# Kernel optimization log

Measured on AMD Instinct MI355X. Metric: run time of the kernel, lower is better.

Reference implementation:

```python
import jax, jax.numpy as jnp
import numpy as np

B, T, DIM, H = 2, 2048, 2048, 16
HD = DIM // H  # 128
ROPE_BASE = 10000.0


def _rope_angles(seq_len, head_dim, offset=0, dtype=jnp.float32):
    inv_freq = 1.0 / (ROPE_BASE ** (jnp.arange(0, head_dim, 2, dtype=dtype) / head_dim))
    pos = jnp.arange(offset, offset + seq_len, dtype=dtype)
    ang = pos[:, None] * inv_freq[None, :]              # [T, HD/2]
    ang = jnp.concatenate([ang, ang], axis=-1)          # [T, HD]
    return jnp.cos(ang), jnp.sin(ang)


def _rotate_half(x):
    x1, x2 = jnp.split(x, 2, axis=-1)
    return jnp.concatenate([-x2, x1], axis=-1)


def setup_inputs() -> dict:
    key = jax.random.key(0)
    ks = jax.random.split(key, 5)
    s = 0.02
    return {
        "x": jax.random.normal(ks[0], (B, T, DIM), dtype=jnp.float32),
        "Wq": jax.random.normal(ks[1], (DIM, DIM), dtype=jnp.float32) * s,
        "Wk": jax.random.normal(ks[2], (DIM, HD), dtype=jnp.float32) * s,
        "Wv": jax.random.normal(ks[3], (DIM, HD), dtype=jnp.float32) * s,
        "Wo": jax.random.normal(ks[4], (DIM, DIM), dtype=jnp.float32) * s,
    }


def reference(x, Wq, Wk, Wv, Wo):
    # q: [B, H, T, HD]; k, v: single shared head [B, T, HD]
    q = (x @ Wq).reshape(B, T, H, HD).transpose(0, 2, 1, 3)
    k = x @ Wk
    v = x @ Wv

    # RoPE (offset=0, no kv cache)
    cos, sin = _rope_angles(T, HD, 0, x.dtype)
    q = q * cos[None, None] + _rotate_half(q) * sin[None, None]
    k = k * cos[None] + _rotate_half(k) * sin[None]

    present_k = k[:, None]  # [B, 1, T, HD]
    present_v = v[:, None]

    # MQA attention: broadcast shared KV head via einsum (no materialized expand)
    scale = 1.0 / jnp.sqrt(jnp.asarray(HD, x.dtype))
    scores = jnp.einsum('bhqd,bkd->bhqk', q, k) * scale  # [B, H, T, T]
    causal = jnp.tril(jnp.ones((T, T), dtype=bool))
    scores = jnp.where(causal[None, None], scores, jnp.finfo(scores.dtype).min)
    attn = jax.nn.softmax(scores, axis=-1)
    out = jnp.einsum('bhqk,bkd->bhqd', attn, v)          # [B, H, T, HD]
    out = out.transpose(0, 2, 1, 3).reshape(B, T, DIM) @ Wo
    return (out, present_k, present_v)
```

## Files before the change

### kernel.cpp

```cpp
#include <hip/hip_runtime.h>


typedef __attribute__((ext_vector_type(8))) short short8;
typedef __attribute__((ext_vector_type(4))) float float4v;
typedef __attribute__((ext_vector_type(4))) unsigned short ushort4v;

#define LOG2E 1.4426950408889634f
#define ATT_SCALE 0.08838834764831845f
#define RLOG 0.20762050593046014f

__device__ __forceinline__ float bf2f(ushort u) {
    union { unsigned u; float f; } v; v.u = ((unsigned)u) << 16; return v.f;
}
__device__ __forceinline__ ushort f2bf(float f) {
    union { float f; unsigned u; } v; v.f = f;
    return (ushort)((v.u + 0x7FFF + ((v.u >> 16) & 1)) >> 16);
}
__device__ __forceinline__ ushort f2bf_fast(float f) {
    union { float f; unsigned u; } v; v.f = f;
    return (ushort)((v.u + 0x8000u) >> 16);
}
__device__ __forceinline__ float4v mfma16(short8 a, short8 b, float4v c) {
    return __builtin_amdgcn_mfma_f32_16x16x32_bf16(a, b, c, 0, 0, 0);
}
__device__ __forceinline__ void gl_lds16(const ushort* g, ushort* l) {
    __builtin_amdgcn_global_load_lds(
        (const __attribute__((address_space(1))) unsigned int*)g,
        (__attribute__((address_space(3))) unsigned int*)l, 16, 0, 0);
}

__global__ __launch_bounds__(256) void prep(const float* __restrict__ x,
                                            ushort* __restrict__ x_bf,
                                            float* __restrict__ tbl) {
    int bid = blockIdx.x;
    if (bid < 512) {
        int idx = bid * 256 + threadIdx.x;
        int d = idx & 63, t = idx >> 6;
        float inv = exp2f(-(float)d * RLOG);
        float s, c;
        sincosf((float)t * inv, &s, &c);
        tbl[idx * 2] = c;  tbl[idx * 2 + 1] = s;
    } else {
        int i = ((bid - 512) * 256 + threadIdx.x) * 4;
        float4v v = *(const float4v*)&x[i];
        ushort4v u;
        #pragma unroll
        for (int r = 0; r < 4; ++r) u[r] = f2bf(v[r]);
        *(ushort4v*)&x_bf[i] = u;
    }
}

__global__ __launch_bounds__(256) void transpose_cvt(const float* __restrict__ in,
                                                     ushort* __restrict__ out,
                                                     int M, int N) {
    __shared__ ushort tile[32][33];
    int cb = blockIdx.x * 32, rb = blockIdx.y * 32;
    int x = threadIdx.x, y0 = threadIdx.y;
    #pragma unroll
    for (int i = 0; i < 32; i += 8)
        tile[y0 + i][x] = f2bf(in[(long)(rb + y0 + i) * N + cb + x]);
    __syncthreads();
    #pragma unroll
    for (int i = 0; i < 32; i += 8)
        out[(long)(cb + y0 + i) * M + rb + x] = tile[x][y0 + i];
}

__global__ __launch_bounds__(256) void transpose_bf16(const ushort* __restrict__ in,
                                                      ushort* __restrict__ out,
                                                      int M, int N) {
    __shared__ ushort tile[32][33];
    int cb = blockIdx.x * 32, rb = blockIdx.y * 32;
    int x = threadIdx.x, y0 = threadIdx.y;
    #pragma unroll
    for (int i = 0; i < 32; i += 8)
        tile[y0 + i][x] = in[(long)(rb + y0 + i) * N + cb + x];
    __syncthreads();
    #pragma unroll
    for (int i = 0; i < 32; i += 8)
        out[(long)(cb + y0 + i) * M + rb + x] = tile[x][y0 + i];
}

__global__ __launch_bounds__(256) void gemm_qkv(const ushort* __restrict__ A,
                                                const ushort* __restrict__ W,
                                                ushort* __restrict__ Cq,
                                                ushort* __restrict__ Ck,
                                                ushort* __restrict__ Cv) {
    constexpr int BM = 128, BN = 128, K = 2048;
    constexpr int SM = 64, SN = 64, MT = 4, NT = 4;
    __shared__ ushort As[BM * 32];
    __shared__ ushort Bs[BN * 32];
    const int m0 = blockIdx.y * BM, n0 = blockIdx.x * BN;
    const int tid = threadIdx.x;
    const int wave = tid >> 6, lane = tid & 63, l15 = lane & 15, quad = lane >> 4;
    const int wr = wave >> 1, wc = wave & 1;

    float4v acc[MT][NT] = {};

    for (int k0 = 0; k0 < K; k0 += 32) {
        __syncthreads();
        #pragma unroll
        for (int p = 0; p < 2; ++p) {
            int lin = (p * 4 + wave) * 64 + lane;
            int row = lin >> 2, c8 = (lin & 3) * 8;
            gl_lds16(&A[(long)(m0 + row) * K + k0 + c8], &As[(p * 4 + wave) * 512]);
        }
        #pragma unroll
        for (int p = 0; p < 2; ++p) {
            int lin = (p * 4 + wave) * 64 + lane;
            int row = lin >> 2, c8 = (lin & 3) * 8;
            gl_lds16(&W[(long)(n0 + row) * K + k0 + c8], &Bs[(p * 4 + wave) * 512]);
        }
        __syncthreads();

        short8 a[MT], b[NT];
        #pragma unroll
        for (int mt = 0; mt < MT; ++mt)
            a[mt] = *(const short8*)&As[(wr * SM + mt * 16 + l15) * 32 + quad * 8];
        #pragma unroll
        for (int nt = 0; nt < NT; ++nt)
            b[nt] = *(const short8*)&Bs[(wc * SN + nt * 16 + l15) * 32 + quad * 8];
        #pragma unroll
        for (int mt = 0; mt < MT; ++mt)
            #pragma unroll
            for (int nt = 0; nt < NT; ++nt)
                acc[mt][nt] = mfma16(a[mt], b[nt], acc[mt][nt]);
    }
    ushort* C;  int Nc, coff;
    if (n0 < 2048)      { C = Cq; Nc = 2048; coff = n0; }
    else if (n0 < 2176) { C = Ck; Nc = 128;  coff = n0 - 2048; }
    else                { C = Cv; Nc = 128;  coff = n0 - 2176; }
    #pragma unroll
    for (int mt = 0; mt < MT; ++mt)
        #pragma unroll
        for (int nt = 0; nt < NT; ++nt)
            #pragma unroll
            for (int r = 0; r < 4; ++r) {
                int row = m0 + wr * SM + mt * 16 + quad * 4 + r;
                int col = coff + wc * SN + nt * 16 + l15;
                C[(long)row * Nc + col] = f2bf(acc[mt][nt][r]);
            }
}

__global__ __launch_bounds__(256) void gemm_out(const ushort* __restrict__ A,
                                                const ushort* __restrict__ W,
                                                float* __restrict__ C) {
    constexpr int BM = 128, BN = 128, K = 2048, N = 2048;
    constexpr int SM = 64, SN = 64, MT = 4, NT = 4;
    __shared__ ushort As[BM * 32];
    __shared__ ushort Bs[BN * 32];
    const int m0 = blockIdx.y * BM, n0 = blockIdx.x * BN;
    const int tid = threadIdx.x;
    const int wave = tid >> 6, lane = tid & 63, l15 = lane & 15, quad = lane >> 4;
    const int wr = wave >> 1, wc = wave & 1;

    float4v acc[MT][NT] = {};

    for (int k0 = 0; k0 < K; k0 += 32) {
        __syncthreads();
        #pragma unroll
        for (int p = 0; p < 2; ++p) {
            int lin = (p * 4 + wave) * 64 + lane;
            int row = lin >> 2, c8 = (lin & 3) * 8;
            gl_lds16(&A[(long)(m0 + row) * K + k0 + c8], &As[(p * 4 + wave) * 512]);
        }
        #pragma unroll
        for (int p = 0; p < 2; ++p) {
            int lin = (p * 4 + wave) * 64 + lane;
            int row = lin >> 2, c8 = (lin & 3) * 8;
            gl_lds16(&W[(long)(n0 + row) * K + k0 + c8], &Bs[(p * 4 + wave) * 512]);
        }
        __syncthreads();

        short8 a[MT], b[NT];
        #pragma unroll
        for (int mt = 0; mt < MT; ++mt)
            a[mt] = *(const short8*)&As[(wr * SM + mt * 16 + l15) * 32 + quad * 8];
        #pragma unroll
        for (int nt = 0; nt < NT; ++nt)
            b[nt] = *(const short8*)&Bs[(wc * SN + nt * 16 + l15) * 32 + quad * 8];
        #pragma unroll
        for (int mt = 0; mt < MT; ++mt)
            #pragma unroll
            for (int nt = 0; nt < NT; ++nt)
                acc[mt][nt] = mfma16(a[mt], b[nt], acc[mt][nt]);
    }
    #pragma unroll
    for (int mt = 0; mt < MT; ++mt)
        #pragma unroll
        for (int nt = 0; nt < NT; ++nt)
            #pragma unroll
            for (int r = 0; r < 4; ++r) {
                int row = m0 + wr * SM + mt * 16 + quad * 4 + r;
                int col = n0 + wc * SN + nt * 16 + l15;
                C[(long)row * N + col] = acc[mt][nt][r];
            }
}

template<int BM, int BN>
__global__ __launch_bounds__(256) void gemm_bt_f32(const float* __restrict__ A32,
                                                   const ushort* __restrict__ B0,
                                                   const ushort* __restrict__ B1,
                                                   ushort* __restrict__ C0,
                                                   ushort* __restrict__ C1,
                                                   int M, int N, int K) {
    constexpr int SM = BM / 2, SN = BN / 2;
    constexpr int MT = SM / 16, NT = SN / 16;
    constexpr int LDK = 40;
    __shared__ ushort As[BM * LDK];
    __shared__ ushort Bs[BN * LDK];
    const ushort* Bm = blockIdx.z ? B1 : B0;
    ushort* C = blockIdx.z ? C1 : C0;
    const int m0 = blockIdx.y * BM, n0 = blockIdx.x * BN;
    const int tid = threadIdx.x;
    const int wave = tid >> 6, lane = tid & 63, l15 = lane & 15, quad = lane >> 4;
    const int wr = wave >> 1, wc = wave & 1;
    float4v acc[MT][NT] = {};
    for (int k0 = 0; k0 < K; k0 += 32) {
        #pragma unroll
        for (int p = 0; p < (BM * 32) / (256 * 4); ++p) {
            int lin = p * 256 + tid;
            int row = lin >> 3, c4 = (lin & 7) * 4;
            float4v v = *(const float4v*)&A32[(long)(m0 + row) * K + k0 + c4];
            ushort4v u;
            #pragma unroll
            for (int i = 0; i < 4; ++i) u[i] = f2bf(v[i]);
            *(ushort4v*)&As[row * LDK + c4] = u;
        }
        #pragma unroll
        for (int p = 0; p < (BN * 4) / 256; ++p) {
            int lin = p * 256 + tid;
            int row = lin >> 2, c8 = (lin & 3) * 8;
            *(short8*)&Bs[row * LDK + c8] =
                *(const short8*)&Bm[(long)(n0 + row) * K + k0 + c8];
        }
        __syncthreads();
        short8 a[MT], b[NT];
        #pragma unroll
        for (int mt = 0; mt < MT; ++mt)
            a[mt] = *(const short8*)&As[(wr * SM + mt * 16 + l15) * LDK + quad * 8];
        #pragma unroll
        for (int nt = 0; nt < NT; ++nt)
            b[nt] = *(const short8*)&Bs[(wc * SN + nt * 16 + l15) * LDK + quad * 8];
        #pragma unroll
        for (int mt = 0; mt < MT; ++mt)
            #pragma unroll
            for (int nt = 0; nt < NT; ++nt)
                acc[mt][nt] = mfma16(a[mt], b[nt], acc[mt][nt]);
        __syncthreads();
    }
    #pragma unroll
    for (int mt = 0; mt < MT; ++mt)
        #pragma unroll
        for (int nt = 0; nt < NT; ++nt)
            #pragma unroll
            for (int r = 0; r < 4; ++r) {
                int row = m0 + wr * SM + mt * 16 + quad * 4 + r;
                int col = n0 + wc * SN + nt * 16 + l15;
                C[(long)row * N + col] = f2bf(acc[mt][nt][r]);
            }
}

__global__ __launch_bounds__(256) void rope_k_present(ushort* __restrict__ Kw,
                                                      const ushort* __restrict__ Vw,
                                                      const float* __restrict__ tbl,
                                                      float* __restrict__ outK,
                                                      float* __restrict__ outV) {
    int idx = blockIdx.x * 256 + threadIdx.x;
    int d = idx & 63;
    int row = idx >> 6;
    int t = row & 2047;
    float c = tbl[(t * 64 + d) * 2], s = tbl[(t * 64 + d) * 2 + 1];
    long base = (long)row * 128 + d;
    float k1 = bf2f(Kw[base]), k2 = bf2f(Kw[base + 64]);
    float r1 = k1 * c - k2 * s, r2 = k2 * c + k1 * s;
    Kw[base] = f2bf(r1);  Kw[base + 64] = f2bf(r2);
    outK[base] = r1;      outK[base + 64] = r2;
    outV[base] = bf2f(Vw[base]); outV[base + 64] = bf2f(Vw[base + 64]);
}

__global__ __launch_bounds__(256, 2) void flash_mqa9(ushort* __restrict__ Q,
                                                     const ushort* __restrict__ Kg,
                                                     const ushort* __restrict__ Vt,
                                                     const float* __restrict__ tbl) {
    constexpr int T = 2048, DIM = 2048;
    constexpr float SCL2 = ATT_SCALE * LOG2E;
    constexpr int LDP = 72;
    __shared__ ushort Ks[2][64 * 128];
    __shared__ ushort Vs[2][128 * 64];
    __shared__ ushort Ps[4][16 * LDP];

    const int i = blockIdx.x;
    int bh, qb;
    if (i < 256) { bh = i >> 3;         qb = 15 - (i & 7); }
    else         { bh = (i - 256) >> 3; qb = i & 7; }
    const int b = bh >> 4, h = bh & 15;
    const int qbase = qb * 128;

    const int tid = threadIdx.x;
    const int wave = tid >> 6, lane = tid & 63, l15 = lane & 15, quad = lane >> 4;
    const int swz = l15 & 7;
    const int qminw = qbase + wave * 32;
    const int nkb = 2 * qb + 2;

    const ushort* kb_ptr = Kg + (long)b * T * 128;
    const ushort* vb_ptr = Vt + (long)b * T;

    int tq[2];
    tq[0] = qminw + l15;
    tq[1] = qminw + 16 + l15;

    short8 qf[2][4];
    #pragma unroll
    for (int qg = 0; qg < 2; ++qg) {
        const ushort* qp = Q + (long)(b * T + tq[qg]) * DIM + h * 128 + quad * 8;
        #pragma unroll
        for (int kc = 0; kc < 4; ++kc) qf[qg][kc] = *(const short8*)(qp + kc * 32);
        #pragma unroll
        for (int kc = 0; kc < 2; ++kc) {
            float ang[16];
            const float4v* tb = (const float4v*)(tbl + ((long)tq[qg] * 64 + kc * 32 + quad * 8) * 2);
            *(float4v*)&ang[0]  = tb[0];
            *(float4v*)&ang[4]  = tb[1];
            *(float4v*)&ang[8]  = tb[2];
            *(float4v*)&ang[12] = tb[3];
            #pragma unroll
            for (int jj = 0; jj < 8; ++jj) {
                float cs = ang[2 * jj] * SCL2, sn = ang[2 * jj + 1] * SCL2;
                float x1 = bf2f((ushort)qf[qg][kc][jj]);
                float x2 = bf2f((ushort)qf[qg][kc + 2][jj]);
                qf[qg][kc][jj]     = (short)f2bf(x1 * cs - x2 * sn);
                qf[qg][kc + 2][jj] = (short)f2bf(x2 * cs + x1 * sn);
            }
        }
    }

    float4v o[2][8] = {};
    float l_part[2] = {0.f, 0.f};

    auto stage = [&](int buf, int t) {
        const int k0 = t * 64;
        #pragma unroll
        for (int p = 0; p < 4; ++p) {
            int ci = (wave * 4 + p) * 64 + lane;
            int kr = ci >> 4, kc = ci & 15;
            gl_lds16(&kb_ptr[(long)(k0 + kr) * 128 + ((kc ^ (kr & 7)) * 8)],
                     &Ks[buf][(wave * 4 + p) * 512]);
            int vd = ci >> 3, vc = ci & 7;
            gl_lds16(&vb_ptr[(long)vd * 4096 + k0 + ((vc ^ (vd & 7)) * 8)],
                     &Vs[buf][(wave * 4 + p) * 512]);
        }
    };

    stage(0, 0);
    __syncthreads();

    for (int t = 0; t < nkb; ++t) {
        const int cur = t & 1;
        if (t + 1 < nkb) stage(cur ^ 1, t + 1);

        const ushort* ksb = &Ks[cur][0];
        const ushort* vsb = &Vs[cur][0];
        const int k0 = t * 64;
        const bool diag = (k0 + 63 > qminw);
        ushort* Pw = &Ps[wave][0];

        #pragma unroll
        for (int qg = 0; qg < 2; ++qg) {
            float4v st[4] = {};
            __builtin_amdgcn_s_setprio(1);
            #pragma unroll
            for (int sub = 0; sub < 4; ++sub) {
                const int r = sub * 16 + l15;
                #pragma unroll
                for (int kc = 0; kc < 4; ++kc) {
                    short8 kf = *(const short8*)&ksb[r * 128 + (((kc * 4 + quad) ^ swz) * 8)];
                    st[sub] = mfma16(kf, qf[qg][kc], st[sub]);
                }
            }
            __builtin_amdgcn_s_setprio(0);

            #pragma unroll
            for (int sub = 0; sub < 4; ++sub) {
                ushort4v pv4;
                #pragma unroll
                for (int rr = 0; rr < 4; ++rr) {
                    float zz = st[sub][rr];
                    if (diag) {
                        int key = k0 + sub * 16 + quad * 4 + rr;
                        zz = (key <= tq[qg]) ? zz : -INFINITY;
                    }
                    float pv = exp2f(zz);
                    l_part[qg] += pv;
                    pv4[rr] = f2bf_fast(pv);
                }
                *(ushort4v*)&Pw[l15 * LDP + sub * 16 + quad * 4] = pv4;
            }

            __builtin_amdgcn_s_setprio(1);
            #pragma unroll
            for (int hf = 0; hf < 2; ++hf) {
                short8 pf = *(const short8*)&Pw[l15 * LDP + hf * 32 + quad * 8];
                #pragma unroll
                for (int nt = 0; nt < 8; ++nt) {
                    short8 vf = *(const short8*)&vsb[(nt * 16 + l15) * 64 + (((hf * 4 + quad) ^ swz) * 8)];
                    o[qg][nt] = mfma16(vf, pf, o[qg][nt]);
                }
            }
            __builtin_amdgcn_s_setprio(0);
        }
        __syncthreads();
    }

    #pragma unroll
    for (int qg = 0; qg < 2; ++qg) {
        float rs = l_part[qg];
        rs += __shfl_xor(rs, 16);
        rs += __shfl_xor(rs, 32);
        float inv_l = 1.0f / rs;
        ushort* dst = Q + (long)(b * T + tq[qg]) * DIM + h * 128;
        #pragma unroll
        for (int nt = 0; nt < 8; ++nt) {
            ushort4v v;
            #pragma unroll
            for (int r = 0; r < 4; ++r) v[r] = f2bf(o[qg][nt][r] * inv_l);
            *(ushort4v*)&dst[nt * 16 + quad * 4] = v;
        }
    }
}

extern "C" void kernel_launch(void* const* d_in, const int* in_sizes, int n_in,
                              void* d_out, int out_size, void* d_ws, size_t ws_size,
                              hipStream_t stream) {
    const float* x  = (const float*)d_in[0];
    const float* Wq = (const float*)d_in[1];
    const float* Wk = (const float*)d_in[2];
    const float* Wv = (const float*)d_in[3];
    const float* Wo = (const float*)d_in[4];
    float* out = (float*)d_out;

    char* ws = (char*)d_ws;
    const bool precast = ws_size >= (46u << 20);
    dim3 tb(32, 8);

    if (precast) {
        ushort* x_bf  = (ushort*)(ws);
        ushort* q_bf  = (ushort*)(ws + (16u << 20));
        ushort* WT    = (ushort*)(ws + (32u << 20));
        ushort* k_bf  = (ushort*)(ws + (42u << 20));
        ushort* v_bf  = (ushort*)(ws + (43u << 20));
        ushort* vt_bf = (ushort*)(ws + (44u << 20));
        float*  ropet = (float*)(ws + (45u << 20));

        prep<<<8704, 256, 0, stream>>>(x, x_bf, ropet);
        transpose_cvt<<<dim3(64, 64), tb, 0, stream>>>(Wq, WT, 2048, 2048);
        transpose_cvt<<<dim3(4, 64),  tb, 0, stream>>>(Wk, WT + (long)2048 * 2048, 2048, 128);
        transpose_cvt<<<dim3(4, 64),  tb, 0, stream>>>(Wv, WT + (long)2176 * 2048, 2048, 128);

        gemm_qkv<<<dim3(18, 32), 256, 0, stream>>>(x_bf, WT, q_bf, k_bf, v_bf);

        rope_k_present<<<1024, 256, 0, stream>>>(k_bf, v_bf, ropet,
                                                 out + 8388608, out + 8912896);
        transpose_bf16<<<dim3(4, 128), tb, 0, stream>>>(v_bf, vt_bf, 4096, 128);

        flash_mqa9<<<512, 256, 0, stream>>>(q_bf, k_bf, vt_bf, ropet);

        transpose_cvt<<<dim3(64, 64), tb, 0, stream>>>(Wo, WT, 2048, 2048);
        gemm_out<<<dim3(16, 32), 256, 0, stream>>>(q_bf, WT, out);
    } else {
        ushort* q_bf  = (ushort*)(ws);
        ushort* WT    = (ushort*)(ws + (16u << 20));
        ushort* k_bf  = (ushort*)(ws + (26u << 20));
        ushort* v_bf  = (ushort*)(ws + (27u << 20));
        ushort* vt_bf = (ushort*)(ws + (28u << 20));
        float*  ropet = (float*)(ws + (29u << 20));
        ushort* WkT = WT + (long)2048 * 2048;
        ushort* WvT = WT + (long)2176 * 2048;

        prep<<<512, 256, 0, stream>>>(x, nullptr, ropet);
        transpose_cvt<<<dim3(64, 64), tb, 0, stream>>>(Wq, WT, 2048, 2048);
        transpose_cvt<<<dim3(4, 64),  tb, 0, stream>>>(Wk, WkT, 2048, 128);
        transpose_cvt<<<dim3(4, 64),  tb, 0, stream>>>(Wv, WvT, 2048, 128);

        gemm_bt_f32<128,128><<<dim3(16, 32, 1), 256, 0, stream>>>(
            x, WT, WT, q_bf, q_bf, 4096, 2048, 2048);
        gemm_bt_f32<64,64><<<dim3(2, 64, 2), 256, 0, stream>>>(
            x, WkT, WvT, k_bf, v_bf, 4096, 128, 2048);

        rope_k_present<<<1024, 256, 0, stream>>>(k_bf, v_bf, ropet,
                                                 out + 8388608, out + 8912896);
        transpose_bf16<<<dim3(4, 128), tb, 0, stream>>>(v_bf, vt_bf, 4096, 128);

        flash_mqa9<<<512, 256, 0, stream>>>(q_bf, k_bf, vt_bf, ropet);

        transpose_cvt<<<dim3(64, 64), tb, 0, stream>>>(Wo, WT, 2048, 2048);
        gemm_out<<<dim3(16, 32), 256, 0, stream>>>(q_bf, WT, out);
    }
}
```

Before: 323.4 us.

## Pair causal q-blocks per workgroup and interleave both query groups in flash MQA

Each workgroup now processes two query blocks (p and 15-p) in sequence, which balances causal work evenly across 256 persistent workgroups instead of 512 uneven ones. Inside the loop, both 16-row query groups share each K and V fragment load, so two MFMA chains run together and LDS reads drop. Waves whose rows lie entirely above a key tile skip that tile's compute. The kernel also drops setprio, and occupancy falls to one workgroup per CU with more registers per thread, so latency hiding may suffer.

```diff
diff --git a/kernel.cpp b/kernel.cpp
--- a/kernel.cpp
+++ b/kernel.cpp
@@ -278,152 +278,157 @@
     outV[base] = bf2f(Vw[base]); outV[base + 64] = bf2f(Vw[base + 64]);
 }
 
-__global__ __launch_bounds__(256, 2) void flash_mqa9(ushort* __restrict__ Q,
-                                                     const ushort* __restrict__ Kg,
-                                                     const ushort* __restrict__ Vt,
-                                                     const float* __restrict__ tbl) {
+__global__ __launch_bounds__(256, 1) void flash_mqa11(ushort* __restrict__ Q,
+                                                      const ushort* __restrict__ Kg,
+                                                      const ushort* __restrict__ Vt,
+                                                      const float* __restrict__ tbl) {
     constexpr int T = 2048, DIM = 2048;
     constexpr float SCL2 = ATT_SCALE * LOG2E;
     constexpr int LDP = 72;
     __shared__ ushort Ks[2][64 * 128];
     __shared__ ushort Vs[2][128 * 64];
-    __shared__ ushort Ps[4][16 * LDP];
-
-    const int i = blockIdx.x;
-    int bh, qb;
-    if (i < 256) { bh = i >> 3;         qb = 15 - (i & 7); }
-    else         { bh = (i - 256) >> 3; qb = i & 7; }
+    __shared__ ushort Ps[4][32 * LDP];
+
+    const int j = blockIdx.x;
+    const int p = j & 7, bh = j >> 3;
     const int b = bh >> 4, h = bh & 15;
-    const int qbase = qb * 128;
 
     const int tid = threadIdx.x;
     const int wave = tid >> 6, lane = tid & 63, l15 = lane & 15, quad = lane >> 4;
     const int swz = l15 & 7;
-    const int qminw = qbase + wave * 32;
-    const int nkb = 2 * qb + 2;
 
     const ushort* kb_ptr = Kg + (long)b * T * 128;
     const ushort* vb_ptr = Vt + (long)b * T;
 
-    int tq[2];
-    tq[0] = qminw + l15;
-    tq[1] = qminw + 16 + l15;
-
-    short8 qf[2][4];
-    #pragma unroll
-    for (int qg = 0; qg < 2; ++qg) {
-        const ushort* qp = Q + (long)(b * T + tq[qg]) * DIM + h * 128 + quad * 8;
-        #pragma unroll
-        for (int kc = 0; kc < 4; ++kc) qf[qg][kc] = *(const short8*)(qp + kc * 32);
-        #pragma unroll
-        for (int kc = 0; kc < 2; ++kc) {
-            float ang[16];
-            const float4v* tb = (const float4v*)(tbl + ((long)tq[qg] * 64 + kc * 32 + quad * 8) * 2);
-            *(float4v*)&ang[0]  = tb[0];
-            *(float4v*)&ang[4]  = tb[1];
-            *(float4v*)&ang[8]  = tb[2];
-            *(float4v*)&ang[12] = tb[3];
-            #pragma unroll
-            for (int jj = 0; jj < 8; ++jj) {
-                float cs = ang[2 * jj] * SCL2, sn = ang[2 * jj + 1] * SCL2;
-                float x1 = bf2f((ushort)qf[qg][kc][jj]);
-                float x2 = bf2f((ushort)qf[qg][kc + 2][jj]);
-                qf[qg][kc][jj]     = (short)f2bf(x1 * cs - x2 * sn);
-                qf[qg][kc + 2][jj] = (short)f2bf(x2 * cs + x1 * sn);
-            }
-        }
-    }
-
-    float4v o[2][8] = {};
-    float l_part[2] = {0.f, 0.f};
-
     auto stage = [&](int buf, int t) {
         const int k0 = t * 64;
         #pragma unroll
-        for (int p = 0; p < 4; ++p) {
-            int ci = (wave * 4 + p) * 64 + lane;
+        for (int pp = 0; pp < 4; ++pp) {
+            int ci = (wave * 4 + pp) * 64 + lane;
             int kr = ci >> 4, kc = ci & 15;
             gl_lds16(&kb_ptr[(long)(k0 + kr) * 128 + ((kc ^ (kr & 7)) * 8)],
-                     &Ks[buf][(wave * 4 + p) * 512]);
+                     &Ks[buf][(wave * 4 + pp) * 512]);
             int vd = ci >> 3, vc = ci & 7;
             gl_lds16(&vb_ptr[(long)vd * 4096 + k0 + ((vc ^ (vd & 7)) * 8)],
-                     &Vs[buf][(wave * 4 + p) * 512]);
+                     &Vs[buf][(wave * 4 + pp) * 512]);
         }
     };
 
-    stage(0, 0);
-    __syncthreads();
-
-    for (int t = 0; t < nkb; ++t) {
-        const int cur = t & 1;
-        if (t + 1 < nkb) stage(cur ^ 1, t + 1);
-
-        const ushort* ksb = &Ks[cur][0];
-        const ushort* vsb = &Vs[cur][0];
-        const int k0 = t * 64;
-        const bool diag = (k0 + 63 > qminw);
-        ushort* Pw = &Ps[wave][0];
-
+    #pragma unroll 1
+    for (int ht = 0; ht < 2; ++ht) {
+        const int qb = ht ? (15 - p) : p;
+        const int qbase = qb * 128;
+        const int qminw = qbase + wave * 32;
+        const int qmaxw = qminw + 31;
+        const int nkb = 2 * (qb + 1);
+
+        int tq[2];
+        tq[0] = qminw + l15;
+        tq[1] = qminw + 16 + l15;
+
+        short8 qf[2][4];
         #pragma unroll
         for (int qg = 0; qg < 2; ++qg) {
-            float4v st[4] = {};
-            __builtin_amdgcn_s_setprio(1);
-            #pragma unroll
-            for (int sub = 0; sub < 4; ++sub) {
-                const int r = sub * 16 + l15;
+            const ushort* qp = Q + (long)(b * T + tq[qg]) * DIM + h * 128 + quad * 8;
+            #pragma unroll
+            for (int kc = 0; kc < 4; ++kc) qf[qg][kc] = *(const short8*)(qp + kc * 32);
+            #pragma unroll
+            for (int kc = 0; kc < 2; ++kc) {
+                float ang[16];
+                const float4v* tb = (const float4v*)(tbl + ((long)tq[qg] * 64 + kc * 32 + quad * 8) * 2);
+                *(float4v*)&ang[0]  = tb[0];
+                *(float4v*)&ang[4]  = tb[1];
+                *(float4v*)&ang[8]  = tb[2];
+                *(float4v*)&ang[12] = tb[3];
                 #pragma unroll
-                for (int kc = 0; kc < 4; ++kc) {
-                    short8 kf = *(const short8*)&ksb[r * 128 + (((kc * 4 + quad) ^ swz) * 8)];
-                    st[sub] = mfma16(kf, qf[qg][kc], st[sub]);
+                for (int jj = 0; jj < 8; ++jj) {
+                    float cs = ang[2 * jj] * SCL2, sn = ang[2 * jj + 1] * SCL2;
+                    float x1 = bf2f((ushort)qf[qg][kc][jj]);
+                    float x2 = bf2f((ushort)qf[qg][kc + 2][jj]);
+                    qf[qg][kc][jj]     = (short)f2bf(x1 * cs - x2 * sn);
+                    qf[qg][kc + 2][jj] = (short)f2bf(x2 * cs + x1 * sn);
                 }
             }
-            __builtin_amdgcn_s_setprio(0);
-
-            #pragma unroll
-            for (int sub = 0; sub < 4; ++sub) {
-                ushort4v pv4;
+        }
+
+        float4v o[2][8] = {};
+        float l_part[2] = {0.f, 0.f};
+
+        stage(0, 0);
+        __syncthreads();
+
+        for (int t = 0; t < nkb; ++t) {
+            const int cur = t & 1;
+            if (t + 1 < nkb) stage(cur ^ 1, t + 1);
+
+            const int k0 = t * 64;
+            if (k0 <= qmaxw) {
+                const ushort* ksb = &Ks[cur][0];
+                const ushort* vsb = &Vs[cur][0];
+
+                float4v st[2][4] = {};
                 #pragma unroll
-                for (int rr = 0; rr < 4; ++rr) {
-                    float zz = st[sub][rr];
-                    if (diag) {
-                        int key = k0 + sub * 16 + quad * 4 + rr;
-                        zz = (key <= tq[qg]) ? zz : -INFINITY;
+                for (int sub = 0; sub < 4; ++sub) {
+                    const int r = sub * 16 + l15;
+                    #pragma unroll
+                    for (int kc = 0; kc < 4; ++kc) {
+                        short8 kf = *(const short8*)&ksb[r * 128 + (((kc * 4 + quad) ^ swz) * 8)];
+                        st[0][sub] = mfma16(kf, qf[0][kc], st[0][sub]);
+                        st[1][sub] = mfma16(kf, qf[1][kc], st[1][sub]);
                     }
-                    float pv = exp2f(zz);
-                    l_part[qg] += pv;
-                    pv4[rr] = f2bf_fast(pv);
                 }
-                *(ushort4v*)&Pw[l15 * LDP + sub * 16 + quad * 4] = pv4;
-            }
-
-            __builtin_amdgcn_s_setprio(1);
-            #pragma unroll
-            for (int hf = 0; hf < 2; ++hf) {
-                short8 pf = *(const short8*)&Pw[l15 * LDP + hf * 32 + quad * 8];
+
+                const bool diag = (k0 + 63 > qminw);
+                ushort* Pw = &Ps[wave][0];
                 #pragma unroll
-                for (int nt = 0; nt < 8; ++nt) {
-                    short8 vf = *(const short8*)&vsb[(nt * 16 + l15) * 64 + (((hf * 4 + quad) ^ swz) * 8)];
-                    o[qg][nt] = mfma16(vf, pf, o[qg][nt]);
+                for (int qg = 0; qg < 2; ++qg) {
+                    #pragma unroll
+                    for (int sub = 0; sub < 4; ++sub) {
+                        ushort4v pv4;
+                        #pragma unroll
+                        for (int rr = 0; rr < 4; ++rr) {
+                            float zz = st[qg][sub][rr];
+                            if (diag) {
+                                int key = k0 + sub * 16 + quad * 4 + rr;
+                                zz = (key <= tq[qg]) ? zz : -INFINITY;
+                            }
+                            float pv = exp2f(zz);
+                            l_part[qg] += pv;
+                            pv4[rr] = f2bf_fast(pv);
+                        }
+                        *(ushort4v*)&Pw[(qg * 16 + l15) * LDP + sub * 16 + quad * 4] = pv4;
+                    }
+                }
+
+                #pragma unroll
+                for (int hf = 0; hf < 2; ++hf) {
+                    short8 pf0 = *(const short8*)&Pw[l15 * LDP + hf * 32 + quad * 8];
+                    short8 pf1 = *(const short8*)&Pw[(16 + l15) * LDP + hf * 32 + quad * 8];
+                    #pragma unroll
+                    for (int nt = 0; nt < 8; ++nt) {
+                        short8 vf = *(const short8*)&vsb[(nt * 16 + l15) * 64 + (((hf * 4 + quad) ^ swz) * 8)];
+                        o[0][nt] = mfma16(vf, pf0, o[0][nt]);
+                        o[1][nt] = mfma16(vf, pf1, o[1][nt]);
+                    }
                 }
             }
-            __builtin_amdgcn_s_setprio(0);
-        }
-        __syncthreads();
-    }
-
-    #pragma unroll
-    for (int qg = 0; qg < 2; ++qg) {
-        float rs = l_part[qg];
-        rs += __shfl_xor(rs, 16);
-        rs += __shfl_xor(rs, 32);
-        float inv_l = 1.0f / rs;
-        ushort* dst = Q + (long)(b * T + tq[qg]) * DIM + h * 128;
-        #pragma unroll
-        for (int nt = 0; nt < 8; ++nt) {
-            ushort4v v;
-            #pragma unroll
-            for (int r = 0; r < 4; ++r) v[r] = f2bf(o[qg][nt][r] * inv_l);
-            *(ushort4v*)&dst[nt * 16 + quad * 4] = v;
+            __syncthreads();
+        }
+
+        #pragma unroll
+        for (int qg = 0; qg < 2; ++qg) {
+            float rs = l_part[qg];
+            rs += __shfl_xor(rs, 16);
+            rs += __shfl_xor(rs, 32);
+            float inv_l = 1.0f / rs;
+            ushort* dst = Q + (long)(b * T + tq[qg]) * DIM + h * 128;
+            #pragma unroll
+            for (int nt = 0; nt < 8; ++nt) {
+                ushort4v v;
+                #pragma unroll
+                for (int r = 0; r < 4; ++r) v[r] = f2bf(o[qg][nt][r] * inv_l);
+                *(ushort4v*)&dst[nt * 16 + quad * 4] = v;
+            }
         }
     }
 }
@@ -462,7 +467,7 @@
                                                  out + 8388608, out + 8912896);
         transpose_bf16<<<dim3(4, 128), tb, 0, stream>>>(v_bf, vt_bf, 4096, 128);
 
-        flash_mqa9<<<512, 256, 0, stream>>>(q_bf, k_bf, vt_bf, ropet);
+        flash_mqa11<<<256, 256, 0, stream>>>(q_bf, k_bf, vt_bf, ropet);
 
         transpose_cvt<<<dim3(64, 64), tb, 0, stream>>>(Wo, WT, 2048, 2048);
         gemm_out<<<dim3(16, 32), 256, 0, stream>>>(q_bf, WT, out);
@@ -490,7 +495,7 @@
                                                  out + 8388608, out + 8912896);
         transpose_bf16<<<dim3(4, 128), tb, 0, stream>>>(v_bf, vt_bf, 4096, 128);
 
-        flash_mqa9<<<512, 256, 0, stream>>>(q_bf, k_bf, vt_bf, ropet);
+        flash_mqa11<<<256, 256, 0, stream>>>(q_bf, k_bf, vt_bf, ropet);
 
         transpose_cvt<<<dim3(64, 64), tb, 0, stream>>>(Wo, WT, 2048, 2048);
         gemm_out<<<dim3(16, 32), 256, 0, stream>>>(q_bf, WT, out);
```

Measured after the change: 318.9 us. About the same (-1.4%).
